# Kernel tuning notes

Measured on AMD Instinct MI355X. Metric: run time of the kernel, lower is better.

## Reference

```python
import jax, jax.numpy as jnp
import numpy as np

SL, BS, D = 2048, 2, 1024
H, DH = 16, 64  # num_heads, nhid

def setup_inputs() -> dict:
    key = jax.random.key(0)
    ks = jax.random.split(key, 8)
    inv = 1.0 / np.sqrt(D)
    return {
        "query": jax.random.normal(ks[0], (SL, BS, D), jnp.float32),
        "keys": jax.random.normal(ks[1], (SL, BS, D), jnp.float32),
        "values": jax.random.normal(ks[2], (SL, BS, D), jnp.float32),
        "mask": jnp.ones((1, 1, SL, SL), jnp.int32),
        "Wq": jax.random.normal(ks[3], (H * DH, D), jnp.float32) * inv,
        "Wk": jax.random.normal(ks[4], (H * DH, D), jnp.float32) * inv,
        "Wv": jax.random.normal(ks[5], (H * DH, D), jnp.float32) * inv,
        "Wo": jax.random.normal(ks[6], (D, H * DH), jnp.float32) * inv,
    }

def reference(query, keys, values, mask, Wq, Wk, Wv, Wo):
    slq, bs, _ = query.shape
    sl = keys.shape[0]
    # nn.Linear(bias=False): x @ W.T ; then view to (s, b, H, DH)
    q = (query @ Wq.T).reshape(slq, bs, H, DH)   # sbhd
    k = (keys @ Wk.T).reshape(sl, bs, H, DH)
    v = (values @ Wv.T).reshape(sl, bs, H, DH)
    # NOTE: original forward never applies self.scale -> unscaled scores.
    scores = jnp.einsum('qbhd,kbhd->bhqk', q, k)
    scores = jnp.where(mask == 0, jnp.float32(-1e20), scores)
    weights = jax.nn.softmax(scores, axis=-1)
    attn = jnp.einsum('bhqk,kbhd->qbhd', weights, v).reshape(slq, bs, H * DH)
    return attn @ Wo.T  # [slq, bs, out_dim]
```

## Files before the change

kernel.cpp:

```cpp
#include <hip/hip_runtime.h>


typedef __attribute__((ext_vector_type(4))) float  f32x4;
typedef __attribute__((ext_vector_type(8))) __bf16 bf16x8;
typedef __attribute__((ext_vector_type(4))) __bf16 bf16x4;

#define SLEN 2048
#define BSZ  2
#define DMODEL 1024
#define NHEAD 16
#define DHEAD 64
#define D3 (3 * DMODEL)

__device__ __forceinline__ void async16(void* lds, const void* g) {
    __builtin_amdgcn_global_load_lds(
        (const __attribute__((address_space(1))) unsigned int*)g,
        (__attribute__((address_space(3))) unsigned int*)lds, 16, 0, 0);
}

__device__ __forceinline__ f32x4 mfma16(bf16x8 a, bf16x8 b, f32x4 c) {
    return __builtin_amdgcn_mfma_f32_16x16x32_bf16(a, b, c, 0, 0, 0);
}

struct CvtArgs {
    const float* src[7];
    __bf16* dst[7];
    int n4[7];
    float scale[7];
    const int* mask;
    unsigned int* flag;
    int maskn4;
};
__global__ void cvt_all(CvtArgs a) {
    const int t = blockIdx.y;
    const int stride = gridDim.x * blockDim.x;
    if (t == 7) {
        bool ok = true;
        for (int i = blockIdx.x * blockDim.x + threadIdx.x; i < a.maskn4; i += stride) {
            int4 v = ((const int4*)a.mask)[i];
            ok = ok && v.x && v.y && v.z && v.w;
        }
        if (!ok) atomicAnd(a.flag, 0u);
        return;
    }
    const float* __restrict__ src = a.src[t];
    __bf16* __restrict__ dst = a.dst[t];
    const int n4 = a.n4[t];
    const float sc = a.scale[t];
    for (int i = blockIdx.x * blockDim.x + threadIdx.x; i < n4; i += stride) {
        float4 v = ((const float4*)src)[i];
        bf16x4 o;
        o[0] = (__bf16)(v.x * sc); o[1] = (__bf16)(v.y * sc);
        o[2] = (__bf16)(v.z * sc); o[3] = (__bf16)(v.w * sc);
        ((bf16x4*)dst)[i] = o;
    }
}

__global__ __launch_bounds__(256, 3) void gemm_qkv(const __bf16* __restrict__ Xq,
                                                   const __bf16* __restrict__ Xk,
                                                   const __bf16* __restrict__ Xv,
                                                   const __bf16* __restrict__ W,
                                                   __bf16* __restrict__ C) {
    __shared__ __bf16 At[128 * 64];
    __shared__ __bf16 Bt[128 * 64];
    const int tid = threadIdx.x;
    const int lane = tid & 63, wv = tid >> 6;
    const int l15 = lane & 15, l4 = lane >> 4;
    const int wr = wv >> 1, wc = wv & 1;
    const int srow = lane >> 3;
    const int sbyte = (((lane & 7) ^ srow) << 4);
    const int bm = blockIdx.x, bn = blockIdx.y;
    const __bf16* A = (bn < 8) ? Xq : (bn < 16) ? Xk : Xv;
    const char* Ab = (const char*)(A + (size_t)bm * 128 * DMODEL);
    const char* Bb = (const char*)(W + (size_t)bn * 128 * DMODEL);

    f32x4 acc[4][4];
#pragma unroll
    for (int m = 0; m < 4; m++)
#pragma unroll
        for (int n = 0; n < 4; n++)
#pragma unroll
            for (int r = 0; r < 4; r++) acc[m][n][r] = 0.0f;

    for (int k0 = 0; k0 < DMODEL; k0 += 64) {
        __syncthreads();
#pragma unroll
        for (int i = 0; i < 8; i++) {
            int c = wv * 8 + i;
            if (c < 16) {
                int row = c * 8 + srow;
                async16(&At[c * 512], Ab + ((size_t)row * DMODEL + k0) * 2 + sbyte);
            } else {
                int row = (c - 16) * 8 + srow;
                async16(&Bt[(c - 16) * 512], Bb + ((size_t)row * DMODEL + k0) * 2 + sbyte);
            }
        }
        __syncthreads();

#pragma unroll
        for (int kk = 0; kk < 2; kk++) {
            bf16x8 af[4], bfr[4];
#pragma unroll
            for (int m = 0; m < 4; m++) {
                int row = wr * 64 + m * 16 + l15;
                int col = (kk * 32 + l4 * 8) ^ ((row & 7) << 3);
                af[m] = *(const bf16x8*)&At[row * 64 + col];
            }
#pragma unroll
            for (int n = 0; n < 4; n++) {
                int row = wc * 64 + n * 16 + l15;
                int col = (kk * 32 + l4 * 8) ^ ((row & 7) << 3);
                bfr[n] = *(const bf16x8*)&Bt[row * 64 + col];
            }
#pragma unroll
            for (int m = 0; m < 4; m++)
#pragma unroll
                for (int n = 0; n < 4; n++)
                    acc[m][n] = mfma16(af[m], bfr[n], acc[m][n]);
        }
    }

#pragma unroll
    for (int m = 0; m < 4; m++)
#pragma unroll
        for (int n = 0; n < 4; n++)
#pragma unroll
            for (int r = 0; r < 4; r++) {
                size_t row = (size_t)bm * 128 + wr * 64 + m * 16 + l4 * 4 + r;
                size_t col = (size_t)bn * 128 + wc * 64 + n * 16 + l15;
                C[row * D3 + col] = (__bf16)acc[m][n][r];
            }
}

__global__ __launch_bounds__(256, 2) void gemm_out(const __bf16* __restrict__ A,
                                                   const __bf16* __restrict__ B,
                                                   float* __restrict__ Cv) {
    __shared__ __bf16 At[2][128 * 64];
    __shared__ __bf16 Bt[2][64 * 64];
    const int tid = threadIdx.x;
    const int lane = tid & 63, wv = tid >> 6;
    const int l15 = lane & 15, l4 = lane >> 4;
    const int wr = wv >> 1, wc = wv & 1;
    const int srow = lane >> 3;
    const int sbyte = (((lane & 7) ^ srow) << 4);
    const int bm = blockIdx.x, bn = blockIdx.y;
    const char* Ab = (const char*)(A + (size_t)bm * 128 * DMODEL);
    const char* Bb = (const char*)(B + (size_t)bn * 64 * DMODEL);

    f32x4 acc[4][2];
#pragma unroll
    for (int m = 0; m < 4; m++)
#pragma unroll
        for (int n = 0; n < 2; n++)
#pragma unroll
            for (int r = 0; r < 4; r++) acc[m][n][r] = 0.0f;

    auto stage = [&](int buf, int k0) {
#pragma unroll
        for (int i = 0; i < 6; i++) {
            int c = wv * 6 + i;
            if (c < 16) {
                int row = c * 8 + srow;
                async16(&At[buf][c * 512], Ab + ((size_t)row * DMODEL + k0) * 2 + sbyte);
            } else {
                int row = (c - 16) * 8 + srow;
                async16(&Bt[buf][(c - 16) * 512], Bb + ((size_t)row * DMODEL + k0) * 2 + sbyte);
            }
        }
    };

    stage(0, 0);
    __syncthreads();
    int cur = 0;
    for (int k0 = 0; k0 < DMODEL; k0 += 64) {
        if (k0 + 64 < DMODEL) stage(cur ^ 1, k0 + 64);
#pragma unroll
        for (int kk = 0; kk < 2; kk++) {
            bf16x8 af[4], bfr[2];
#pragma unroll
            for (int m = 0; m < 4; m++) {
                int row = wr * 64 + m * 16 + l15;
                int col = (kk * 32 + l4 * 8) ^ ((row & 7) << 3);
                af[m] = *(const bf16x8*)&At[cur][row * 64 + col];
            }
#pragma unroll
            for (int n = 0; n < 2; n++) {
                int row = wc * 32 + n * 16 + l15;
                int col = (kk * 32 + l4 * 8) ^ ((row & 7) << 3);
                bfr[n] = *(const bf16x8*)&Bt[cur][row * 64 + col];
            }
#pragma unroll
            for (int m = 0; m < 4; m++)
#pragma unroll
                for (int n = 0; n < 2; n++)
                    acc[m][n] = mfma16(af[m], bfr[n], acc[m][n]);
        }
        __syncthreads();
        cur ^= 1;
    }

#pragma unroll
    for (int m = 0; m < 4; m++)
#pragma unroll
        for (int n = 0; n < 2; n++)
#pragma unroll
            for (int r = 0; r < 4; r++) {
                size_t row = (size_t)bm * 128 + wr * 64 + m * 16 + l4 * 4 + r;
                size_t col = (size_t)bn * 64 + wc * 32 + n * 16 + l15;
                Cv[row * DMODEL + col] = acc[m][n][r];
            }
}

__global__ __launch_bounds__(256) void transpose_v(const __bf16* __restrict__ QKV,
                                                   __bf16* __restrict__ Vt) {
    __shared__ __bf16 t[64][72];
    const int stile = blockIdx.x;
    const int bh = blockIdx.y;
    const int b = bh >> 4, h = bh & 15;
    const int tid = threadIdx.x;
    {
        int sr = tid >> 2, d0 = (tid & 3) * 16;
        const __bf16* src = QKV + ((size_t)((stile * 64 + sr) * BSZ + b) * D3 + 2 * DMODEL + h * 64 + d0);
        *(bf16x8*)&t[sr][d0]     = *(const bf16x8*)src;
        *(bf16x8*)&t[sr][d0 + 8] = *(const bf16x8*)(src + 8);
    }
    __syncthreads();
    {
        int d = tid >> 2, s0 = (tid & 3) * 16;
        bf16x8 o1, o2;
#pragma unroll
        for (int j = 0; j < 8; j++) { o1[j] = t[s0 + j][d]; o2[j] = t[s0 + 8 + j][d]; }
        __bf16* dst = Vt + ((size_t)(bh * 64 + d) * SLEN + stile * 64 + s0);
        *(bf16x8*)dst = o1;
        *(bf16x8*)(dst + 8) = o2;
    }
}

__global__ __launch_bounds__(256, 2) void attn_fwd(const __bf16* __restrict__ QKV,
                                                   const __bf16* __restrict__ Vt,
                                                   const int* __restrict__ mask,
                                                   const unsigned int* __restrict__ flag,
                                                   __bf16* __restrict__ Attn) {
    __shared__ __bf16 Kt[2][2][64 * 64];
    __shared__ __bf16 Vs[2][2][64 * 64];
    const int tid = threadIdx.x;
    const int lane = tid & 63, wv = tid >> 6;
    const int l15 = lane & 15, l4 = lane >> 4;
    const int blk = blockIdx.x;
    const int xcd = blk & 7, idx = blk >> 3;
    const int bh = xcd + (idx >> 4) * 8;
    const int qt = idx & 15;
    const int b = bh >> 4, h = bh & 15;
    const bool allones = (*flag != 0u);
    const int srow = lane >> 3;
    const int sbyte = (((lane & 7) ^ srow) << 4);

    bf16x8 aq[2][2];
#pragma unroll
    for (int m = 0; m < 2; m++)
#pragma unroll
        for (int kk = 0; kk < 2; kk++) {
            int qrow = qt * 128 + wv * 32 + m * 16 + l15;
            aq[m][kk] = *(const bf16x8*)(QKV + ((size_t)(qrow * BSZ + b) * D3 + h * 64 + kk * 32 + l4 * 8));
        }

    f32x4 o[2][4];
    float lr[2];
#pragma unroll
    for (int m = 0; m < 2; m++) {
#pragma unroll
        for (int nd = 0; nd < 4; nd++)
#pragma unroll
            for (int r = 0; r < 4; r++) o[m][nd][r] = 0.0f;
        lr[m] = 0.0f;
    }

    const char* Kb = (const char*)QKV + ((size_t)b * D3 + DMODEL + h * 64) * 2;
    const char* Vb = (const char*)Vt + ((size_t)bh * 64) * SLEN * 2;

    auto stage = [&](int buf, int kt) {
#pragma unroll
        for (int i = 0; i < 8; i++) {
            int c = wv * 8 + i;
            if (c < 16) {
                int kh = c >> 3, ck = c & 7;
                int p = (ck & 7) * 8 + srow;
                int kperm = (p & 32) + ((p & 12) << 1) + (((p >> 4) & 1) << 2) + (p & 3);
                int krow = kt * 128 + kh * 64 + kperm;
                async16(&Kt[buf][kh][ck * 512],
                        Kb + (size_t)krow * (BSZ * D3 * 2) + sbyte);
            } else {
                int c2 = c - 16;
                int kh = c2 >> 3, ck = c2 & 7;
                int drow = ck * 8 + srow;
                async16(&Vs[buf][kh][ck * 512],
                        Vb + (size_t)drow * (SLEN * 2) + kt * 256 + kh * 128 + sbyte);
            }
        }
    };

    stage(0, 0);
    __syncthreads();
    int cur = 0;

    for (int kt = 0; kt < SLEN / 128; kt++) {
        if (kt + 1 < SLEN / 128) stage(cur ^ 1, kt + 1);

#pragma unroll
        for (int kh = 0; kh < 2; kh++) {
            const __bf16* Kl = Kt[cur][kh];
            const __bf16* Vl = Vs[cur][kh];

            bf16x8 bk[4][2];
#pragma unroll
            for (int n = 0; n < 4; n++) {
                int row = n * 16 + l15;
#pragma unroll
                for (int kk = 0; kk < 2; kk++) {
                    int col = (kk * 32 + l4 * 8) ^ ((row & 7) << 3);
                    bk[n][kk] = *(const bf16x8*)&Kl[row * 64 + col];
                }
            }

            f32x4 s[2][4];
#pragma unroll
            for (int m = 0; m < 2; m++)
#pragma unroll
                for (int n = 0; n < 4; n++)
#pragma unroll
                    for (int r = 0; r < 4; r++) s[m][n][r] = 0.0f;
            __builtin_amdgcn_s_setprio(1);
#pragma unroll
            for (int n = 0; n < 4; n++)
#pragma unroll
                for (int kk = 0; kk < 2; kk++)
#pragma unroll
                    for (int m = 0; m < 2; m++)
                        s[m][n] = mfma16(bk[n][kk], aq[m][kk], s[m][n]);
            __builtin_amdgcn_s_setprio(0);

            if (!allones) {
#pragma unroll
                for (int m = 0; m < 2; m++) {
                    int q = qt * 128 + wv * 32 + m * 16 + l15;
#pragma unroll
                    for (int n = 0; n < 4; n++)
#pragma unroll
                        for (int r = 0; r < 4; r++) {
                            int kg = kt * 128 + kh * 64 + (n >> 1) * 32 + l4 * 8 + (n & 1) * 4 + r;
                            if (mask[(size_t)q * SLEN + kg] == 0) s[m][n][r] = -1e20f;
                        }
                }
            }

            bf16x8 pb8[2][2];
#pragma unroll
            for (int m = 0; m < 2; m++)
#pragma unroll
                for (int half = 0; half < 2; half++)
#pragma unroll
                    for (int nn = 0; nn < 2; nn++)
#pragma unroll
                        for (int r = 0; r < 4; r++) {
                            float p = __builtin_amdgcn_exp2f(s[m][half * 2 + nn][r]);
                            lr[m] += p;
                            pb8[m][half][nn * 4 + r] = (__bf16)p;
                        }

            __builtin_amdgcn_s_setprio(1);
#pragma unroll
            for (int half = 0; half < 2; half++) {
#pragma unroll
                for (int nd = 0; nd < 4; nd++) {
                    int row = nd * 16 + l15;
                    int col = (half * 32 + l4 * 8) ^ ((row & 7) << 3);
                    bf16x8 av = *(const bf16x8*)&Vl[row * 64 + col];
#pragma unroll
                    for (int m = 0; m < 2; m++)
                        o[m][nd] = mfma16(av, pb8[m][half], o[m][nd]);
                }
            }
            __builtin_amdgcn_s_setprio(0);
        }

        __syncthreads();
        cur ^= 1;
    }

#pragma unroll
    for (int m = 0; m < 2; m++) {
        lr[m] += __shfl_xor(lr[m], 16);
        lr[m] += __shfl_xor(lr[m], 32);
    }

#pragma unroll
    for (int m = 0; m < 2; m++) {
        float inv = 1.0f / lr[m];
        int qrow = qt * 128 + wv * 32 + m * 16 + l15;
#pragma unroll
        for (int nd = 0; nd < 4; nd++) {
            bf16x4 ov;
#pragma unroll
            for (int r = 0; r < 4; r++) ov[r] = (__bf16)(o[m][nd][r] * inv);
            *(bf16x4*)(Attn + ((size_t)(qrow * BSZ + b)) * DMODEL + h * 64 + nd * 16 + l4 * 4) = ov;
        }
    }
}

extern "C" void kernel_launch(void* const* d_in, const int* in_sizes, int n_in,
                              void* d_out, int out_size, void* d_ws, size_t ws_size,
                              hipStream_t stream) {
    const float* query  = (const float*)d_in[0];
    const float* keys   = (const float*)d_in[1];
    const float* values = (const float*)d_in[2];
    const int*   mask   = (const int*)d_in[3];
    const float* Wq     = (const float*)d_in[4];
    const float* Wk     = (const float*)d_in[5];
    const float* Wv     = (const float*)d_in[6];
    const float* Wo     = (const float*)d_in[7];
    float* out = (float*)d_out;

    char* ws = (char*)d_ws;
    const size_t MB = 1024 * 1024;
    __bf16* XQ   = (__bf16*)(ws + 0);
    __bf16* XK   = (__bf16*)(ws + 8 * MB);
    __bf16* XV   = (__bf16*)(ws + 16 * MB);
    __bf16* WCAT = (__bf16*)(ws + 24 * MB);
    __bf16* WQB  = WCAT;
    __bf16* WKB  = (__bf16*)(ws + 26 * MB);
    __bf16* WVB  = (__bf16*)(ws + 28 * MB);
    __bf16* WOB  = (__bf16*)(ws + 30 * MB);
    __bf16* QKV  = (__bf16*)(ws + 32 * MB);
    __bf16* VT   = (__bf16*)(ws + 0);
    __bf16* ATT  = (__bf16*)(ws + 8 * MB);
    unsigned int* flag = (unsigned int*)(ws + 56 * MB);

    (void)hipMemsetAsync(flag, 0xFF, 4, stream);

    const int NTOK = SLEN * BSZ;
    const int NBIG = NTOK * DMODEL / 4, NW = DMODEL * DMODEL / 4;
    const float LOG2E = 1.4426950408889634f;
    CvtArgs ca;
    ca.src[0] = query;  ca.dst[0] = XQ;  ca.n4[0] = NBIG; ca.scale[0] = 1.0f;
    ca.src[1] = keys;   ca.dst[1] = XK;  ca.n4[1] = NBIG; ca.scale[1] = 1.0f;
    ca.src[2] = values; ca.dst[2] = XV;  ca.n4[2] = NBIG; ca.scale[2] = 1.0f;
    ca.src[3] = Wq;     ca.dst[3] = WQB; ca.n4[3] = NW;   ca.scale[3] = LOG2E;
    ca.src[4] = Wk;     ca.dst[4] = WKB; ca.n4[4] = NW;   ca.scale[4] = 1.0f;
    ca.src[5] = Wv;     ca.dst[5] = WVB; ca.n4[5] = NW;   ca.scale[5] = 1.0f;
    ca.src[6] = Wo;     ca.dst[6] = WOB; ca.n4[6] = NW;   ca.scale[6] = 1.0f;
    ca.mask = mask; ca.flag = flag; ca.maskn4 = SLEN * SLEN / 4;
    cvt_all<<<dim3(256, 8), 256, 0, stream>>>(ca);

    gemm_qkv<<<dim3(NTOK / 128, D3 / 128), 256, 0, stream>>>(XQ, XK, XV, WCAT, QKV);

    transpose_v<<<dim3(SLEN / 64, BSZ * NHEAD), 256, 0, stream>>>(QKV, VT);

    attn_fwd<<<BSZ * NHEAD * (SLEN / 128), 256, 0, stream>>>(QKV, VT, mask, flag, ATT);

    gemm_out<<<dim3(NTOK / 128, DMODEL / 64), 256, 0, stream>>>(ATT, WOB, out);
}
```

Baseline: 122.9 us.

## Fuse V transpose into QKV GEMM epilogue and compute row sums via MFMA

The QKV GEMM now writes Q/K to a packed buffer and writes V directly in transposed per-head layout, which removes the separate transpose kernel and its extra pass over V. In attention, softmax denominators are accumulated with an extra MFMA against a vector of ones instead of scalar adds plus cross-lane shuffles. The cost is scattered, poorly coalesced global stores for the V tiles and a few extra matrix instructions per tile.

```diff
diff --git a/kernel.cpp b/kernel.cpp
--- a/kernel.cpp
+++ b/kernel.cpp
@@ -10,7 +10,7 @@
 #define DMODEL 1024
 #define NHEAD 16
 #define DHEAD 64
-#define D3 (3 * DMODEL)
+#define D2 (2 * DMODEL)
 
 __device__ __forceinline__ void async16(void* lds, const void* g) {
     __builtin_amdgcn_global_load_lds(
@@ -60,7 +60,8 @@
                                                    const __bf16* __restrict__ Xk,
                                                    const __bf16* __restrict__ Xv,
                                                    const __bf16* __restrict__ W,
-                                                   __bf16* __restrict__ C) {
+                                                   __bf16* __restrict__ QK,
+                                                   __bf16* __restrict__ VT) {
     __shared__ __bf16 At[128 * 64];
     __shared__ __bf16 Bt[128 * 64];
     const int tid = threadIdx.x;
@@ -120,16 +121,30 @@
         }
     }
 
-#pragma unroll
-    for (int m = 0; m < 4; m++)
-#pragma unroll
-        for (int n = 0; n < 4; n++)
-#pragma unroll
-            for (int r = 0; r < 4; r++) {
-                size_t row = (size_t)bm * 128 + wr * 64 + m * 16 + l4 * 4 + r;
-                size_t col = (size_t)bn * 128 + wc * 64 + n * 16 + l15;
-                C[row * D3 + col] = (__bf16)acc[m][n][r];
-            }
+    if (bn < 16) {
+#pragma unroll
+        for (int m = 0; m < 4; m++)
+#pragma unroll
+            for (int n = 0; n < 4; n++)
+#pragma unroll
+                for (int r = 0; r < 4; r++) {
+                    size_t row = (size_t)bm * 128 + wr * 64 + m * 16 + l4 * 4 + r;
+                    size_t col = (size_t)bn * 128 + wc * 64 + n * 16 + l15;
+                    QK[row * D2 + col] = (__bf16)acc[m][n][r];
+                }
+    } else {
+#pragma unroll
+        for (int m = 0; m < 4; m++)
+#pragma unroll
+            for (int n = 0; n < 4; n++)
+#pragma unroll
+                for (int r = 0; r < 4; r++) {
+                    int t = bm * 128 + wr * 64 + m * 16 + l4 * 4 + r;
+                    int hd = (bn - 16) * 128 + wc * 64 + n * 16 + l15;
+                    int s = t >> 1, b = t & 1;
+                    VT[((size_t)(b * NHEAD * DHEAD + hd)) * SLEN + s] = (__bf16)acc[m][n][r];
+                }
+    }
 }
 
 __global__ __launch_bounds__(256, 2) void gemm_out(const __bf16* __restrict__ A,
@@ -211,32 +226,7 @@
             }
 }
 
-__global__ __launch_bounds__(256) void transpose_v(const __bf16* __restrict__ QKV,
-                                                   __bf16* __restrict__ Vt) {
-    __shared__ __bf16 t[64][72];
-    const int stile = blockIdx.x;
-    const int bh = blockIdx.y;
-    const int b = bh >> 4, h = bh & 15;
-    const int tid = threadIdx.x;
-    {
-        int sr = tid >> 2, d0 = (tid & 3) * 16;
-        const __bf16* src = QKV + ((size_t)((stile * 64 + sr) * BSZ + b) * D3 + 2 * DMODEL + h * 64 + d0);
-        *(bf16x8*)&t[sr][d0]     = *(const bf16x8*)src;
-        *(bf16x8*)&t[sr][d0 + 8] = *(const bf16x8*)(src + 8);
-    }
-    __syncthreads();
-    {
-        int d = tid >> 2, s0 = (tid & 3) * 16;
-        bf16x8 o1, o2;
-#pragma unroll
-        for (int j = 0; j < 8; j++) { o1[j] = t[s0 + j][d]; o2[j] = t[s0 + 8 + j][d]; }
-        __bf16* dst = Vt + ((size_t)(bh * 64 + d) * SLEN + stile * 64 + s0);
-        *(bf16x8*)dst = o1;
-        *(bf16x8*)(dst + 8) = o2;
-    }
-}
-
-__global__ __launch_bounds__(256, 2) void attn_fwd(const __bf16* __restrict__ QKV,
+__global__ __launch_bounds__(256, 2) void attn_fwd(const __bf16* __restrict__ QK,
                                                    const __bf16* __restrict__ Vt,
                                                    const int* __restrict__ mask,
                                                    const unsigned int* __restrict__ flag,
@@ -261,21 +251,25 @@
 #pragma unroll
         for (int kk = 0; kk < 2; kk++) {
             int qrow = qt * 128 + wv * 32 + m * 16 + l15;
-            aq[m][kk] = *(const bf16x8*)(QKV + ((size_t)(qrow * BSZ + b) * D3 + h * 64 + kk * 32 + l4 * 8));
-        }
-
-    f32x4 o[2][4];
-    float lr[2];
+            aq[m][kk] = *(const bf16x8*)(QK + ((size_t)(qrow * BSZ + b) * D2 + h * 64 + kk * 32 + l4 * 8));
+        }
+
+    bf16x8 ones;
+#pragma unroll
+    for (int j = 0; j < 8; j++) ones[j] = (__bf16)1.0f;
+
+    f32x4 o[2][4], olr[2];
 #pragma unroll
     for (int m = 0; m < 2; m++) {
 #pragma unroll
         for (int nd = 0; nd < 4; nd++)
 #pragma unroll
             for (int r = 0; r < 4; r++) o[m][nd][r] = 0.0f;
-        lr[m] = 0.0f;
-    }
-
-    const char* Kb = (const char*)QKV + ((size_t)b * D3 + DMODEL + h * 64) * 2;
+#pragma unroll
+        for (int r = 0; r < 4; r++) olr[m][r] = 0.0f;
+    }
+
+    const char* Kb = (const char*)QK + ((size_t)b * D2 + DMODEL + h * 64) * 2;
     const char* Vb = (const char*)Vt + ((size_t)bh * 64) * SLEN * 2;
 
     auto stage = [&](int buf, int kt) {
@@ -288,7 +282,7 @@
                 int kperm = (p & 32) + ((p & 12) << 1) + (((p >> 4) & 1) << 2) + (p & 3);
                 int krow = kt * 128 + kh * 64 + kperm;
                 async16(&Kt[buf][kh][ck * 512],
-                        Kb + (size_t)krow * (BSZ * D3 * 2) + sbyte);
+                        Kb + (size_t)krow * (BSZ * D2 * 2) + sbyte);
             } else {
                 int c2 = c - 16;
                 int kh = c2 >> 3, ck = c2 & 7;
@@ -363,7 +357,6 @@
 #pragma unroll
                         for (int r = 0; r < 4; r++) {
                             float p = __builtin_amdgcn_exp2f(s[m][half * 2 + nn][r]);
-                            lr[m] += p;
                             pb8[m][half][nn * 4 + r] = (__bf16)p;
                         }
 
@@ -379,6 +372,9 @@
                     for (int m = 0; m < 2; m++)
                         o[m][nd] = mfma16(av, pb8[m][half], o[m][nd]);
                 }
+#pragma unroll
+                for (int m = 0; m < 2; m++)
+                    olr[m] = mfma16(ones, pb8[m][half], olr[m]);
             }
             __builtin_amdgcn_s_setprio(0);
         }
@@ -389,13 +385,7 @@
 
 #pragma unroll
     for (int m = 0; m < 2; m++) {
-        lr[m] += __shfl_xor(lr[m], 16);
-        lr[m] += __shfl_xor(lr[m], 32);
-    }
-
-#pragma unroll
-    for (int m = 0; m < 2; m++) {
-        float inv = 1.0f / lr[m];
+        float inv = 1.0f / olr[m][0];
         int qrow = qt * 128 + wv * 32 + m * 16 + l15;
 #pragma unroll
         for (int nd = 0; nd < 4; nd++) {
@@ -430,8 +420,8 @@
     __bf16* WKB  = (__bf16*)(ws + 26 * MB);
     __bf16* WVB  = (__bf16*)(ws + 28 * MB);
     __bf16* WOB  = (__bf16*)(ws + 30 * MB);
-    __bf16* QKV  = (__bf16*)(ws + 32 * MB);
-    __bf16* VT   = (__bf16*)(ws + 0);
+    __bf16* QKB  = (__bf16*)(ws + 32 * MB);
+    __bf16* VT   = (__bf16*)(ws + 48 * MB);
     __bf16* ATT  = (__bf16*)(ws + 8 * MB);
     unsigned int* flag = (unsigned int*)(ws + 56 * MB);
 
@@ -451,11 +441,9 @@
     ca.mask = mask; ca.flag = flag; ca.maskn4 = SLEN * SLEN / 4;
     cvt_all<<<dim3(256, 8), 256, 0, stream>>>(ca);
 
-    gemm_qkv<<<dim3(NTOK / 128, D3 / 128), 256, 0, stream>>>(XQ, XK, XV, WCAT, QKV);
-
-    transpose_v<<<dim3(SLEN / 64, BSZ * NHEAD), 256, 0, stream>>>(QKV, VT);
-
-    attn_fwd<<<BSZ * NHEAD * (SLEN / 128), 256, 0, stream>>>(QKV, VT, mask, flag, ATT);
+    gemm_qkv<<<dim3(NTOK / 128, 3 * DMODEL / 128), 256, 0, stream>>>(XQ, XK, XV, WCAT, QKB, VT);
+
+    attn_fwd<<<BSZ * NHEAD * (SLEN / 128), 256, 0, stream>>>(QKB, VT, mask, flag, ATT);
 
     gemm_out<<<dim3(NTOK / 128, DMODEL / 64), 256, 0, stream>>>(ATT, WOB, out);
 }
```

After: 118.9 us, median of 2. 1.03x faster.
